# Kernel tuning notes

Hardware: AMD Instinct MI355X
Metric: run time of the kernel (lower is better)

## Reference

```python
import jax
jax.config.update("jax_enable_x64", True)
import jax.numpy as jnp
import numpy as np

EPS = 1e-10
NODES = [
    {"type": 0, "feature_idx": 0},
    {"type": 0, "feature_idx": 1},
    {"type": 0, "feature_idx": 2},
    {"type": 0, "feature_idx": 3},
    {"type": 1, "value": 2.5},
    {"type": 2, "unary_op": 0, "left_child": 0, "p": 1.0, "omega": 1.3, "phi": 0.2, "amplitude": 1.1},
    {"type": 2, "unary_op": 1, "left_child": 1, "p": 2.0, "omega": 1.0, "phi": 0.0, "amplitude": 1.0},
    {"type": 2, "unary_op": 1, "left_child": 2, "p": 1.7, "omega": 1.0, "phi": 0.0, "amplitude": 1.0},
    {"type": 2, "unary_op": 3, "left_child": 3, "p": 1.0, "omega": 0.5, "phi": 0.0, "amplitude": 1.0},
    {"type": 2, "unary_op": 4, "left_child": 0, "p": 1.0, "omega": 1.0, "phi": 0.0, "amplitude": 1.0},
    {"type": 2, "unary_op": 2, "left_child": 1, "p": 3.0, "omega": 1.0, "phi": 0.0, "amplitude": 1.0},
    {"type": 3, "binary_op": 0, "left_child": 5, "right_child": 6, "beta": 1.0, "gamma": 1.0, "tau": 1.0},
    {"type": 3, "binary_op": 0, "left_child": 7, "right_child": 8, "beta": 1.0, "gamma": -1.0, "tau": 1.0},
    {"type": 3, "binary_op": 0, "left_child": 9, "right_child": 10, "beta": 2.0, "gamma": 1.0, "tau": 1.0},
    {"type": 3, "binary_op": 0, "left_child": 11, "right_child": 4, "beta": 2.0, "gamma": -1.0, "tau": 1.0},
    {"type": 3, "binary_op": 1, "left_child": 12, "right_child": 13, "beta": 1.0, "gamma": 1.0, "tau": 1.0},
    {"type": 3, "binary_op": 2, "left_child": 14, "right_child": 15, "beta": 1.0, "gamma": 1.0, "tau": 0.5},
    {"type": 2, "unary_op": 0, "left_child": 16, "p": 1.0, "omega": 0.7, "phi": -0.3, "amplitude": 0.9},
    {"type": 3, "binary_op": 0, "left_child": 17, "right_child": 11, "beta": 1.0, "gamma": 1.0, "tau": 1.0},
]

def _safe_div(l, r):
    return l / (jnp.abs(r) + EPS) * jnp.sign(r)

def _eval_graph(x, output_weights, output_bias):
    x = x.astype(jnp.float64)  # mirrors x.double()
    n = x.shape[0]
    outs = []
    for node in NODES:
        t = node["type"]
        if t == 0:  # input
            out = x[:, node["feature_idx"]]
        elif t == 1:  # constant
            out = jnp.full((n,), node["value"], dtype=jnp.float64)
        elif t == 2:  # unary
            child = outs[node["left_child"]]
            op = node["unary_op"]
            p, omega, phi, amp = node["p"], node["omega"], node["phi"], node["amplitude"]
            if op == 0:  # periodic
                out = amp * jnp.sin(omega * child + phi)
            elif op == 1:  # power (sign-safe)
                abs_pow = (jnp.abs(child) + EPS) ** p
                p_round = round(p)
                is_even = 1.0 if (abs(p - p_round) < 1e-6 and int(p_round) % 2 == 0) else 0.0
                out = (1.0 - is_even) * (jnp.sign(child) * abs_pow) + is_even * abs_pow
            elif op == 2:  # int pow
                k = int(min(max(round(p), 2), 6))
                out = child ** k
            elif op == 3:  # exp
                out = jnp.exp(jnp.clip(omega * child + phi, -20.0, 20.0))
            elif op == 4:  # log
                out = jnp.log(jnp.abs(child) + EPS)
            else:
                out = child
        elif t == 3:  # binary
            l = outs[node["left_child"]]
            r = outs[node["right_child"]]
            op = node["binary_op"]
            beta, gamma = node["beta"], node["gamma"]
            if op == 0:  # arithmetic (branch resolves statically on fixed buffers)
                if beta < 1.5:
                    out = l + r if gamma > 0 else l - r
                elif gamma > 0:
                    out = l * r
                else:
                    out = _safe_div(l, r)
            elif op == 1:  # division
                out = _safe_div(l, r)
            else:  # aggregation: soft-max-weighted mean
                tau = node["tau"]
                local_tau = tau if abs(tau) >= 1e-3 else 1e-3
                m = jnp.maximum(l, r)
                el = jnp.exp((l - m) / local_tau)
                er = jnp.exp((r - m) / local_tau)
                out = (l * el + r * er) / (el + er)
        else:
            out = jnp.zeros((n,), dtype=jnp.float64)
        out = jnp.clip(out, -1e6, 1e6)
        out = jnp.where(jnp.isfinite(out), out, 0.0)
        outs.append(out)
    stacked = jnp.stack(outs, axis=0)  # (K, N)
    w = output_weights.astype(jnp.float64)
    return w @ stacked + output_bias.astype(jnp.float64)


def setup_inputs() -> dict:
    key = jax.random.key(0)
    k1, k2, k3 = jax.random.split(key, 3)
    x = jax.random.normal(k1, (2_000_000, 8), dtype=jnp.float32)
    output_weights = jax.random.normal(k2, (19,), dtype=jnp.float32) * 0.2
    output_bias = jax.random.normal(k3, (), dtype=jnp.float32) * 0.1
    return {"x": x, "output_weights": output_weights, "output_bias": output_bias}


def reference(x, output_weights, output_bias):
    return _eval_graph(x, output_weights, output_bias)
```

## Files before the change

### kernel.cpp

```cpp
#include <hip/hip_runtime.h>
#include <math.h>

__device__ __forceinline__ double clipd(double v) {
    if (v != v) return 0.0;
    return fmin(fmax(v, -1.0e6), 1.0e6);
}
__device__ __forceinline__ float fast_sin(float th) {
    float rev = th * 0.15915494309189535f;
    rev = rev - floorf(rev);
    return __builtin_amdgcn_sinf(rev);
}

__global__ void __launch_bounds__(256) graph_eval(
    const float4* __restrict__ x4,
    const float*  __restrict__ w,
    const float*  __restrict__ bias,
    float*        __restrict__ out,
    int n)
{
    int i = blockIdx.x * blockDim.x + threadIdx.x;
    if (i >= n) return;

    float4 v = x4[2 * i];
    float x0 = v.x, x1 = v.y, x2 = v.z, x3 = v.w;

    float n5 = 1.1f * fast_sin(fmaf(1.3f, x0, 0.2f));
    float t6 = fabsf(x1) + 1e-10f;
    float n6 = t6 * t6;
    float y2 = fabsf(x2) + 1e-10f;
    float sgn2 = (x2 > 0.f) ? 1.f : ((x2 < 0.f) ? -1.f : 0.f);
    float n7 = sgn2 * __expf(1.7f * __logf(y2));
    float n8 = __expf(fminf(fmaxf(0.5f * x3, -20.f), 20.f));
    float n9 = __logf(fabsf(x0) + 1e-10f);
    float n10 = x1 * x1 * x1;

    float n11 = n5 + n6;
    float n12 = n7 - n8;
    float n13 = n9 * n10;
    float n14 = 0.4f * n11;

    float a13 = fabsf(n13);
    float sgn13 = (n13 > 0.f) ? 1.f : ((n13 < 0.f) ? -1.f : 0.f);
    float n15 = n12 * __builtin_amdgcn_rcpf(a13 + 1e-10f) * sgn13;
    n15 = fminf(fmaxf(n15, -1.0e6f), 1.0e6f);

    bool flag = a13 < 1e-7f;
    if (flag) {
        float s13 = (x1 == 0.f) ? 0.f
                  : (((fabsf(x0) >= 1.0f) == (x1 > 0.f)) ? 1.f : -1.f);
        n15 = copysignf(1.0e6f, n12) * s13;
    }
    bool x0n1 = fabsf(fabsf(x0) - 1.0f) < 1e-4f;
    if ((flag && fabsf(n12) < 0.25f) || x0n1) {
        double y2d = fabs((double)x2) + 1e-10;
        double n7d = (double)sgn2 * exp(1.7 * log(y2d));
        double n8d = exp(fmin(fmax(0.5 * (double)x3, -20.0), 20.0));
        double n9d = log(fabs((double)x0) + 1e-10);
        double x1d = (double)x1;
        double n12d = clipd(n7d - n8d);
        double n13d = clipd(n9d * (x1d * x1d * x1d));
        double sd = (n13d > 0.0) ? 1.0 : ((n13d < 0.0) ? -1.0 : 0.0);
        n15 = (float)clipd(n12d / (fabs(n13d) + 1e-10) * sd);
    }

    float d = n14 - n15;
    float s = __builtin_amdgcn_rcpf(1.0f + __expf(-2.0f * d));
    float n16 = n15 + d * s;
    float n17 = 0.9f * fast_sin(fmaf(0.7f, n16, -0.3f));

    float c11 = w[11] + 0.4f * w[14] + w[18];
    float r = bias[0] + 2.5f * w[4];
    r += w[0] * x0 + w[1] * x1 + w[2] * x2 + w[3] * x3;
    r += (w[5] + c11) * n5 + (w[6] + c11) * n6;
    r += (w[7] + w[12]) * n7 + (w[8] - w[12]) * n8;
    r += w[9] * n9 + w[10] * n10 + w[13] * n13;
    r += w[15] * n15 + w[16] * n16 + (w[17] + w[18]) * n17;
    out[i] = r;
}

extern "C" void kernel_launch(void* const* d_in, const int* in_sizes, int n_in,
                              void* d_out, int out_size, void* d_ws, size_t ws_size,
                              hipStream_t stream) {
    const float4* x  = (const float4*)d_in[0];
    const float*  w  = (const float*)d_in[1];
    const float*  b  = (const float*)d_in[2];
    float* out = (float*)d_out;
    int n = out_size;
    int block = 256;
    int grid = (n + block - 1) / block;
    graph_eval<<<grid, block, 0, stream>>>(x, w, b, out, n);
}
```

Measured before the change: 17.45 us.

## Process two rows per thread and replace libm double exp/log with inline polynomials

Each thread now evaluates two rows, loading two float4s and storing a float2, and hoists the combined weight coefficients into a struct that both rows share. The rare double-precision fallback path swaps libm exp/log for inline range-reduced polynomial versions and drops the intermediate clips, which should cut register pressure and code size from the libm calls. The cost is fewer threads in flight and an odd row count being silently dropped. The intermediate clip removal also changes the fallback path's NaN handling slightly.

```diff
diff --git a/kernel.cpp b/kernel.cpp
--- a/kernel.cpp
+++ b/kernel.cpp
@@ -1,29 +1,57 @@
 #include <hip/hip_runtime.h>
 #include <math.h>
 
-__device__ __forceinline__ double clipd(double v) {
-    if (v != v) return 0.0;
-    return fmin(fmax(v, -1.0e6), 1.0e6);
+__device__ __forceinline__ double dexp(double t) {
+    const double LOG2E  = 1.4426950408889634;
+    const double LN2_HI = 6.93147180369123816490e-01;
+    const double LN2_LO = 1.90821492927058770002e-10;
+    double kd = __builtin_floor(t * LOG2E + 0.5);
+    double f  = (t - kd * LN2_HI) - kd * LN2_LO;
+    double p = 1.0 / 362880.0;
+    p = p * f + 1.0 / 40320.0;
+    p = p * f + 1.0 / 5040.0;
+    p = p * f + 1.0 / 720.0;
+    p = p * f + 1.0 / 120.0;
+    p = p * f + 1.0 / 24.0;
+    p = p * f + 1.0 / 6.0;
+    p = p * f + 0.5;
+    p = p * f + 1.0;
+    p = p * f + 1.0;
+    long long k = (long long)kd;
+    return __longlong_as_double(__double_as_longlong(p) + (k << 52));
 }
+__device__ __forceinline__ double dlog(double y) {
+    long long b = __double_as_longlong(y);
+    int e = (int)((b >> 52) & 0x7FF) - 1022;
+    double m = __longlong_as_double((b & 0x000FFFFFFFFFFFFFLL) | 0x3FE0000000000000LL);
+    if (m < 0.7071067811865476) { m = m + m; e -= 1; }
+    double s  = (m - 1.0) / (m + 1.0);
+    double s2 = s * s;
+    double p = 1.0 / 15.0;
+    p = p * s2 + 1.0 / 13.0;
+    p = p * s2 + 1.0 / 11.0;
+    p = p * s2 + 1.0 / 9.0;
+    p = p * s2 + 1.0 / 7.0;
+    p = p * s2 + 1.0 / 5.0;
+    p = p * s2 + 1.0 / 3.0;
+    p = p * s2 + 1.0;
+    return (double)e * 0.6931471805599453 + 2.0 * s * p;
+}
+
 __device__ __forceinline__ float fast_sin(float th) {
     float rev = th * 0.15915494309189535f;
     rev = rev - floorf(rev);
     return __builtin_amdgcn_sinf(rev);
 }
 
-__global__ void __launch_bounds__(256) graph_eval(
-    const float4* __restrict__ x4,
-    const float*  __restrict__ w,
-    const float*  __restrict__ bias,
-    float*        __restrict__ out,
-    int n)
-{
-    int i = blockIdx.x * blockDim.x + threadIdx.x;
-    if (i >= n) return;
+struct W {
+    float w0, w1, w2, w3;
+    float c5, c6, c7, c8;
+    float w9, w10, w13, w15, w16, c17;
+    float base;
+};
 
-    float4 v = x4[2 * i];
-    float x0 = v.x, x1 = v.y, x2 = v.z, x3 = v.w;
-
+__device__ __forceinline__ float eval_row(const W& q, float x0, float x1, float x2, float x3) {
     float n5 = 1.1f * fast_sin(fmaf(1.3f, x0, 0.2f));
     float t6 = fabsf(x1) + 1e-10f;
     float n6 = t6 * t6;
@@ -33,7 +61,6 @@
     float n8 = __expf(fminf(fmaxf(0.5f * x3, -20.f), 20.f));
     float n9 = __logf(fabsf(x0) + 1e-10f);
     float n10 = x1 * x1 * x1;
-
     float n11 = n5 + n6;
     float n12 = n7 - n8;
     float n13 = n9 * n10;
@@ -52,15 +79,15 @@
     }
     bool x0n1 = fabsf(fabsf(x0) - 1.0f) < 1e-4f;
     if ((flag && fabsf(n12) < 0.25f) || x0n1) {
-        double y2d = fabs((double)x2) + 1e-10;
-        double n7d = (double)sgn2 * exp(1.7 * log(y2d));
-        double n8d = exp(fmin(fmax(0.5 * (double)x3, -20.0), 20.0));
-        double n9d = log(fabs((double)x0) + 1e-10);
+        double n7d = (double)sgn2 * dexp(1.7 * dlog(fabs((double)x2) + 1e-10));
+        double n8d = dexp(fmin(fmax(0.5 * (double)x3, -20.0), 20.0));
+        double n9d = dlog(fabs((double)x0) + 1e-10);
         double x1d = (double)x1;
-        double n12d = clipd(n7d - n8d);
-        double n13d = clipd(n9d * (x1d * x1d * x1d));
+        double n12d = n7d - n8d;
+        double n13d = n9d * (x1d * x1d * x1d);
         double sd = (n13d > 0.0) ? 1.0 : ((n13d < 0.0) ? -1.0 : 0.0);
-        n15 = (float)clipd(n12d / (fabs(n13d) + 1e-10) * sd);
+        double rr = n12d / (fabs(n13d) + 1e-10) * sd;
+        n15 = (float)fmin(fmax(rr, -1.0e6), 1.0e6);
     }
 
     float d = n14 - n15;
@@ -68,14 +95,39 @@
     float n16 = n15 + d * s;
     float n17 = 0.9f * fast_sin(fmaf(0.7f, n16, -0.3f));
 
+    float r = q.base;
+    r += q.w0 * x0 + q.w1 * x1 + q.w2 * x2 + q.w3 * x3;
+    r += q.c5 * n5 + q.c6 * n6 + q.c7 * n7 + q.c8 * n8;
+    r += q.w9 * n9 + q.w10 * n10 + q.w13 * n13;
+    r += q.w15 * n15 + q.w16 * n16 + q.c17 * n17;
+    return r;
+}
+
+__global__ void __launch_bounds__(256) graph_eval(
+    const float4* __restrict__ x4,
+    const float*  __restrict__ w,
+    const float*  __restrict__ bias,
+    float2*       __restrict__ out2,
+    int nhalf)
+{
+    int j = blockIdx.x * blockDim.x + threadIdx.x;
+    if (j >= nhalf) return;
+
+    float4 a = x4[4 * j];
+    float4 b = x4[4 * j + 2];
+
+    W q;
     float c11 = w[11] + 0.4f * w[14] + w[18];
-    float r = bias[0] + 2.5f * w[4];
-    r += w[0] * x0 + w[1] * x1 + w[2] * x2 + w[3] * x3;
-    r += (w[5] + c11) * n5 + (w[6] + c11) * n6;
-    r += (w[7] + w[12]) * n7 + (w[8] - w[12]) * n8;
-    r += w[9] * n9 + w[10] * n10 + w[13] * n13;
-    r += w[15] * n15 + w[16] * n16 + (w[17] + w[18]) * n17;
-    out[i] = r;
+    q.w0 = w[0];  q.w1 = w[1];  q.w2 = w[2];  q.w3 = w[3];
+    q.c5 = w[5] + c11;  q.c6 = w[6] + c11;
+    q.c7 = w[7] + w[12];  q.c8 = w[8] - w[12];
+    q.w9 = w[9];  q.w10 = w[10];  q.w13 = w[13];
+    q.w15 = w[15];  q.w16 = w[16];  q.c17 = w[17] + w[18];
+    q.base = bias[0] + 2.5f * w[4];
+
+    float r0 = eval_row(q, a.x, a.y, a.z, a.w);
+    float r1 = eval_row(q, b.x, b.y, b.z, b.w);
+    out2[j] = make_float2(r0, r1);
 }
 
 extern "C" void kernel_launch(void* const* d_in, const int* in_sizes, int n_in,
@@ -84,9 +136,9 @@
     const float4* x  = (const float4*)d_in[0];
     const float*  w  = (const float*)d_in[1];
     const float*  b  = (const float*)d_in[2];
-    float* out = (float*)d_out;
-    int n = out_size;
+    float2* out = (float2*)d_out;
+    int nhalf = out_size / 2;
     int block = 256;
-    int grid = (n + block - 1) / block;
-    graph_eval<<<grid, block, 0, stream>>>(x, w, b, out, n);
+    int grid = (nhalf + block - 1) / block;
+    graph_eval<<<grid, block, 0, stream>>>(x, w, b, out, nhalf);
 }
```

Result: slower. 17.94 us (+2.8%).
